# Kernel tuning notes

Hardware: AMD Instinct MI355X
Metric: run time of the kernel (lower is better)

Reference implementation:

```python
import jax, jax.numpy as jnp
import numpy as np

B, N, C, H, R = 16, 1024, 768, 12, 16
HD = C // H
SCALE = HD ** -0.5


def setup_inputs() -> dict:
    key = jax.random.key(0)
    ks = jax.random.split(key, 13)
    f = lambda k, shape, s=0.02: jax.random.normal(k, shape, dtype=jnp.float32) * s
    return {
        "x": jax.random.normal(ks[0], (B, N, C), dtype=jnp.float32),
        "W_qkv": f(ks[1], (3 * C, C)),
        "b_qkv": f(ks[2], (3 * C,)),
        "W_proj": f(ks[3], (C, C)),
        "b_proj": f(ks[4], (C,)),
        "A_q": f(ks[5], (R, C)),
        "B_q": f(ks[6], (C, R)),
        "A_k": f(ks[7], (R, C)),
        "B_k": f(ks[8], (C, R)),
        "A_v": f(ks[9], (R, C)),
        "B_v": f(ks[10], (C, R)),
        "A_o": f(ks[11], (R, C)),
        "B_o": f(ks[12], (C, R)),
    }


def _lora(x, A, Bu):
    # Adapter with no norm/act/bias, scaling=1.0: low-rank x @ A^T @ B^T
    return (x @ A.T) @ Bu.T


def _heads(t):
    # [B, N, C] -> [B, H, N, HD]
    return t.reshape(B, N, H, HD).transpose(0, 2, 1, 3)


def reference(x, W_qkv, b_qkv, W_proj, b_proj, A_q, B_q, A_k, B_k, A_v, B_v, A_o, B_o):
    qkv = x @ W_qkv.T + b_qkv                    # [B, N, 3C]
    qkv = qkv.reshape(B, N, 3, H, HD).transpose(2, 0, 3, 1, 4)  # [3, B, H, N, HD]
    q, k, v = qkv[0], qkv[1], qkv[2]
    q = q + _heads(_lora(x, A_q, B_q))
    k = k + _heads(_lora(x, A_k, B_k))
    v = v + _heads(_lora(x, A_v, B_v))
    attn = jnp.einsum("bhnd,bhmd->bhnm", q, k) * SCALE
    attn = jax.nn.softmax(attn, axis=-1)
    out = jnp.einsum("bhnm,bhmd->bhnd", attn, v)  # [B, H, N, HD]
    out = out.transpose(0, 2, 1, 3).reshape(B, N, C)
    out = out @ W_proj.T + b_proj
    out = out + _lora(out, A_o, B_o)
    return out
```

## Files before the change

kernel.cpp:

```cpp
#include <hip/hip_runtime.h>
#include <cmath>


#define DEVI __device__ __forceinline__

typedef float f32x4 __attribute__((ext_vector_type(4)));
typedef float f32x16 __attribute__((ext_vector_type(16)));
typedef short s16x8 __attribute__((ext_vector_type(8)));
typedef __bf16 b16x8 __attribute__((ext_vector_type(8)));
typedef unsigned int u32x4 __attribute__((ext_vector_type(4)));

static constexpr int MTOT = 16384;
static constexpr int C = 768;
static constexpr int N3 = 2304;

DEVI unsigned short f2bf(float x) {
  unsigned int u = __builtin_bit_cast(unsigned int, x);
  return (unsigned short)((u + 0x7FFFu + ((u >> 16) & 1u)) >> 16);
}

DEVI f32x4 mfma16(s16x8 a, s16x8 b, f32x4 c) {
  return __builtin_amdgcn_mfma_f32_16x16x32_bf16(
      __builtin_bit_cast(b16x8, a), __builtin_bit_cast(b16x8, b), c, 0, 0, 0);
}

DEVI f32x16 mfma32(s16x8 a, s16x8 b, f32x16 c) {
  return __builtin_amdgcn_mfma_f32_32x32x16_bf16(
      __builtin_bit_cast(b16x8, a), __builtin_bit_cast(b16x8, b), c, 0, 0, 0);
}

DEVI void async16(const void* g, void* l) {
  __builtin_amdgcn_global_load_lds(
      (__attribute__((address_space(1))) void*)g,
      (__attribute__((address_space(3))) void*)l, 16, 0, 0);
}

DEVI unsigned cvtpk_bf16(float lo, float hi2) {
  unsigned r;
  asm("v_cvt_pk_bf16_f32 %0, %1, %2" : "=v"(r) : "v"(lo), "v"(hi2));
  return r;
}


__global__ __launch_bounds__(256) void k_prep_x(const float* __restrict__ x,
                                                unsigned short* __restrict__ xb) {
  int idx = (blockIdx.x * 256 + threadIdx.x) * 4;
  float4 v = *(const float4*)(x + idx);
  uint2 p;
  p.x = (unsigned int)f2bf(v.x) | ((unsigned int)f2bf(v.y) << 16);
  p.y = (unsigned int)f2bf(v.z) | ((unsigned int)f2bf(v.w) << 16);
  *(uint2*)(xb + idx) = p;
}

__global__ __launch_bounds__(256) void k_prep_wqkv(
    const float* __restrict__ W, const float* __restrict__ Aq,
    const float* __restrict__ Bq, const float* __restrict__ Ak,
    const float* __restrict__ Bk, const float* __restrict__ Av,
    const float* __restrict__ Bv, unsigned short* __restrict__ out) {
  int idx = blockIdx.x * 256 + threadIdx.x;
  int n = idx / 768, c = idx - n * 768;
  int s = n / 768, co = n - s * 768;
  const float* A = (s == 0) ? Aq : (s == 1) ? Ak : Av;
  const float* Bm = (s == 0) ? Bq : (s == 1) ? Bk : Bv;
  float acc = W[idx];
#pragma unroll
  for (int r = 0; r < 16; ++r) acc += Bm[co * 16 + r] * A[r * 768 + c];
  out[idx] = f2bf(acc);
}

__global__ __launch_bounds__(256) void k_prep_M(const float* __restrict__ Ao,
                                                const float* __restrict__ Wp,
                                                float* __restrict__ M) {
  __shared__ float red[4][64];
  const int r = blockIdx.x, j0 = blockIdx.y * 64;
  const int jl = threadIdx.x & 63, cs = threadIdx.x >> 6;
  float acc = 0.f;
#pragma unroll 4
  for (int c = cs * 192; c < cs * 192 + 192; ++c)
    acc += Ao[r * 768 + c] * Wp[c * 768 + j0 + jl];
  red[cs][jl] = acc;
  __syncthreads();
  if (cs == 0)
    M[r * 768 + j0 + jl] = red[0][jl] + red[1][jl] + red[2][jl] + red[3][jl];
}

__global__ __launch_bounds__(256) void k_prep_wpe(const float* __restrict__ Wp,
                                                  const float* __restrict__ Bo,
                                                  const float* __restrict__ M,
                                                  unsigned short* __restrict__ out) {
  int idx = blockIdx.x * 256 + threadIdx.x;
  int n = idx / 768, j = idx - n * 768;
  float acc = Wp[idx];
#pragma unroll
  for (int r = 0; r < 16; ++r) acc += Bo[n * 16 + r] * M[r * 768 + j];
  out[idx] = f2bf(acc);
}

__global__ __launch_bounds__(256) void k_prep_beff(const float* __restrict__ bp,
                                                   const float* __restrict__ Ao,
                                                   const float* __restrict__ Bo,
                                                   float* __restrict__ beff) {
  __shared__ float red[256];
  __shared__ float bv[16];
  const int t = threadIdx.x;
  const int r = t >> 4, cs = t & 15;
  float a = 0.f;
#pragma unroll 4
  for (int c = cs * 48; c < cs * 48 + 48; ++c) a += Ao[r * 768 + c] * bp[c];
  red[t] = a;
  __syncthreads();
  if (cs == 0) {
    float s = 0.f;
#pragma unroll
    for (int k = 0; k < 16; ++k) s += red[r * 16 + k];
    bv[r] = s;
  }
  __syncthreads();
#pragma unroll
  for (int it = 0; it < 3; ++it) {
    const int n = it * 256 + t;
    float acc = bp[n];
#pragma unroll
    for (int r2 = 0; r2 < 16; ++r2) acc += Bo[n * 16 + r2] * bv[r2];
    beff[n] = acc;
  }
}


template <bool SWAP>
__global__ __launch_bounds__(256) void k_gemm_qkv_t(
    const unsigned short* __restrict__ A, const unsigned short* __restrict__ Bw,
    const float* __restrict__ bias, int nblk0, unsigned short* __restrict__ qb,
    unsigned short* __restrict__ kb, unsigned short* __restrict__ vtb) {
  __shared__ short la[2][128 * 32];
  __shared__ short lb[2][128 * 32];
  const int t = threadIdx.x;
  const int w = t >> 6, l = t & 63;
  const int i = l & 15, qd = l >> 4;
  const int wm = w >> 1, wn = w & 1;
  const int mblk = blockIdx.x, nblk = nblk0 + blockIdx.y;

  const unsigned short* Ab = A + (size_t)(mblk * 128) * 768;
  const unsigned short* Bb = Bw + (size_t)(nblk * 128) * 768;
  const int sr = l >> 2;
  const int sc = (l & 3) * 8;

  auto stage = [&](int bufn, int kb_) {
    const int k0 = kb_ * 32;
#pragma unroll
    for (int j = 0; j < 2; ++j) {
      const int row = w * 32 + j * 16 + sr;
      async16(Ab + row * 768 + k0 + sc, &la[bufn][(w * 32 + j * 16) * 32]);
      async16(Bb + row * 768 + k0 + sc, &lb[bufn][(w * 32 + j * 16) * 32]);
    }
  };

  stage(0, 0);

  f32x4 acc[4][4] = {};

  for (int kb_ = 0; kb_ < 24; ++kb_) {
    const int buf = kb_ & 1;
    __syncthreads();
    if (kb_ < 23) stage(buf ^ 1, kb_ + 1);
    s16x8 af[4], bf[4];
#pragma unroll
    for (int mi = 0; mi < 4; ++mi)
      af[mi] = *(const s16x8*)&la[buf][(wm * 64 + mi * 16 + i) * 32 + qd * 8];
#pragma unroll
    for (int ni = 0; ni < 4; ++ni)
      bf[ni] = *(const s16x8*)&lb[buf][(wn * 64 + ni * 16 + i) * 32 + qd * 8];
#pragma unroll
    for (int mi = 0; mi < 4; ++mi)
#pragma unroll
      for (int ni = 0; ni < 4; ++ni) {
        if constexpr (SWAP)
          acc[mi][ni] = mfma16(bf[ni], af[mi], acc[mi][ni]);
        else
          acc[mi][ni] = mfma16(af[mi], bf[ni], acc[mi][ni]);
      }
  }

  const float c1 = 0.18033688011112042f;
  if constexpr (SWAP) {
#pragma unroll
    for (int ni = 0; ni < 4; ++ni) {
      const int n0 = nblk * 128 + wn * 64 + ni * 16 + qd * 4;
      const int s = n0 / 768;
      const int nrel = n0 - s * 768;
      const int h = nrel >> 6, d0 = nrel & 63;
      const float4 bv4 = *(const float4*)(bias + n0);
      unsigned short* dst = (s == 0) ? qb : kb;
      const float scl = (s == 0) ? c1 : 1.0f;
#pragma unroll
      for (int mi = 0; mi < 4; ++mi) {
        const int m = mblk * 128 + wm * 64 + mi * 16 + i;
        const int b = m >> 10, pos = m & 1023;
        uint2 pk;
        pk.x = (unsigned int)f2bf((acc[mi][ni][0] + bv4.x) * scl) |
               ((unsigned int)f2bf((acc[mi][ni][1] + bv4.y) * scl) << 16);
        pk.y = (unsigned int)f2bf((acc[mi][ni][2] + bv4.z) * scl) |
               ((unsigned int)f2bf((acc[mi][ni][3] + bv4.w) * scl) << 16);
        *(uint2*)&dst[(size_t)((b * 12 + h) * 1024 + pos) * 64 + d0] = pk;
      }
    }
  } else {
#pragma unroll
    for (int ni = 0; ni < 4; ++ni) {
      const int n = nblk * 128 + wn * 64 + ni * 16 + i;
      const int nrel = n - 1536;
      const int h = nrel >> 6, d = nrel & 63;
      const float bvv = bias[n];
#pragma unroll
      for (int mi = 0; mi < 4; ++mi) {
        const int m0 = mblk * 128 + wm * 64 + mi * 16 + qd * 4;
        const int b = m0 >> 10, pos0 = m0 & 1023;
        uint2 pk;
        pk.x = (unsigned int)f2bf(acc[mi][ni][0] + bvv) |
               ((unsigned int)f2bf(acc[mi][ni][1] + bvv) << 16);
        pk.y = (unsigned int)f2bf(acc[mi][ni][2] + bvv) |
               ((unsigned int)f2bf(acc[mi][ni][3] + bvv) << 16);
        *(uint2*)&vtb[(size_t)((b * 12 + h) * 64 + d) * 1024 + pos0] = pk;
      }
    }
  }
}


__global__ __launch_bounds__(256, 4) void k_attn(
    const unsigned short* __restrict__ qg, const unsigned short* __restrict__ kg,
    const unsigned short* __restrict__ vtg, unsigned short* __restrict__ og) {
  __shared__ short k_lds[2][64 * 64];
  __shared__ short vt_lds[2][64 * 64];

  const int t = threadIdx.x;
  const int w = t >> 6, l = t & 63;
  const int lc = l & 31;
  const int hi = l >> 5;
  const int bh = blockIdx.x;
  const int qblk = blockIdx.y;
  const int h = bh % 12, b = bh / 12;

  const unsigned short* Qg = qg + (size_t)(bh * 1024 + qblk * 128) * 64;
  const unsigned short* Kg = kg + (size_t)bh * 1024 * 64;
  const unsigned short* Vtg = vtg + (size_t)bh * 64 * 1024;

  const int srl = l >> 3;
  const int sgc = (l & 7) ^ srl;

  s16x8 qf[4];
#pragma unroll
  for (int kc = 0; kc < 4; ++kc)
    qf[kc] = *(const s16x8*)(Qg + (w * 32 + lc) * 64 + kc * 16 + hi * 8);

  int koffs[2][4];
#pragma unroll
  for (int pg = 0; pg < 2; ++pg)
#pragma unroll
    for (int kc = 0; kc < 4; ++kc)
      koffs[pg][kc] = (pg * 32 + lc) * 64 + (((kc * 2 + hi) ^ (lc & 7)) * 8);
  int voffs[2][4][2];
#pragma unroll
  for (int nd = 0; nd < 2; ++nd)
#pragma unroll
    for (int mi = 0; mi < 4; ++mi)
#pragma unroll
      for (int h2 = 0; h2 < 2; ++h2)
        voffs[nd][mi][h2] =
            (nd * 32 + lc) * 64 + (((2 * mi + h2) ^ (lc & 7)) * 8) + 4 * hi;

  auto stage = [&](int bufn, int tkv) {
#pragma unroll
    for (int it = 0; it < 2; ++it) {
      const int rbase = it * 32 + w * 8;
      async16(Kg + (size_t)(tkv * 64 + rbase + srl) * 64 + sgc * 8,
              &k_lds[bufn][rbase * 64]);
      async16(Vtg + (size_t)(rbase + srl) * 1024 + tkv * 64 + sgc * 8,
              &vt_lds[bufn][rbase * 64]);
    }
  };

  stage(0, 0);

  f32x16 oacc[2] = {};
  float llocal = 0.f;

  for (int tkv = 0; tkv < 16; ++tkv) {
    const int buf = tkv & 1;
    __syncthreads();
    if (tkv < 15) stage(buf ^ 1, tkv + 1);

#pragma unroll
    for (int pg = 0; pg < 2; ++pg) {
      f32x16 st = {};
#pragma unroll
      for (int kc = 0; kc < 4; ++kc) {
        const s16x8 ka = *(const s16x8*)&k_lds[buf][koffs[pg][kc]];
        st = mfma32(ka, qf[kc], st);
      }
      unsigned pk[4][2];
#pragma unroll
      for (int q = 0; q < 4; ++q) {
        const float e0 = __builtin_amdgcn_exp2f(st[4 * q + 0]);
        const float e1 = __builtin_amdgcn_exp2f(st[4 * q + 1]);
        const float e2 = __builtin_amdgcn_exp2f(st[4 * q + 2]);
        const float e3 = __builtin_amdgcn_exp2f(st[4 * q + 3]);
        pk[q][0] = cvtpk_bf16(e0, e1);
        pk[q][1] = cvtpk_bf16(e2, e3);
        llocal += (e0 + e1) + (e2 + e3);
      }
      __builtin_amdgcn_s_setprio(1);
#pragma unroll
      for (int m = 0; m < 2; ++m) {
        const int mi = pg * 2 + m;
        u32x4 fa;
        fa[0] = pk[2 * m][0];
        fa[1] = pk[2 * m][1];
        fa[2] = pk[2 * m + 1][0];
        fa[3] = pk[2 * m + 1][1];
        const s16x8 paf = __builtin_bit_cast(s16x8, fa);
#pragma unroll
        for (int nd = 0; nd < 2; ++nd) {
          const uint2 vlo = *(const uint2*)&vt_lds[buf][voffs[nd][mi][0]];
          const uint2 vhi = *(const uint2*)&vt_lds[buf][voffs[nd][mi][1]];
          u32x4 vbu;
          vbu[0] = vlo.x;
          vbu[1] = vlo.y;
          vbu[2] = vhi.x;
          vbu[3] = vhi.y;
          oacc[nd] = mfma32(paf, __builtin_bit_cast(s16x8, vbu), oacc[nd]);
        }
      }
      __builtin_amdgcn_s_setprio(0);
    }
  }

  const float lq = llocal + __shfl_xor(llocal, 32, 64);
  float linv[16];
#pragma unroll
  for (int r = 0; r < 16; ++r)
    linv[r] = 1.0f / __shfl(lq, (r & 3) + 8 * (r >> 2) + 4 * hi, 64);

  const int orow0 = qblk * 128 + w * 32;
#pragma unroll
  for (int nd = 0; nd < 2; ++nd)
#pragma unroll
    for (int r = 0; r < 16; ++r) {
      const int pos = orow0 + (r & 3) + 8 * (r >> 2) + 4 * hi;
      const int d = nd * 32 + lc;
      og[(size_t)(b * 1024 + pos) * 768 + h * 64 + d] = f2bf(oacc[nd][r] * linv[r]);
    }
}


__global__ __launch_bounds__(256) void k_gemm_proj(
    const unsigned short* __restrict__ A, const unsigned short* __restrict__ Bw,
    const float* __restrict__ bias, float* __restrict__ out) {
  __shared__ short la[2][128 * 32];
  __shared__ short lb[2][128 * 32];
  const int t = threadIdx.x;
  const int w = t >> 6, l = t & 63;
  const int i = l & 15, qd = l >> 4;
  const int wm = w >> 1, wn = w & 1;
  const int mblk = blockIdx.x, nblk = blockIdx.y;

  const unsigned short* Ab = A + (size_t)(mblk * 128) * 768;
  const unsigned short* Bb = Bw + (size_t)(nblk * 128) * 768;
  const int sr = l >> 2;
  const int sc = (l & 3) * 8;

  auto stage = [&](int bufn, int kb_) {
    const int k0 = kb_ * 32;
#pragma unroll
    for (int j = 0; j < 2; ++j) {
      const int row = w * 32 + j * 16 + sr;
      async16(Ab + row * 768 + k0 + sc, &la[bufn][(w * 32 + j * 16) * 32]);
      async16(Bb + row * 768 + k0 + sc, &lb[bufn][(w * 32 + j * 16) * 32]);
    }
  };

  stage(0, 0);

  f32x4 acc[4][4] = {};

  for (int kb_ = 0; kb_ < 24; ++kb_) {
    const int buf = kb_ & 1;
    __syncthreads();
    if (kb_ < 23) stage(buf ^ 1, kb_ + 1);
    s16x8 af[4], bf[4];
#pragma unroll
    for (int mi = 0; mi < 4; ++mi)
      af[mi] = *(const s16x8*)&la[buf][(wm * 64 + mi * 16 + i) * 32 + qd * 8];
#pragma unroll
    for (int ni = 0; ni < 4; ++ni)
      bf[ni] = *(const s16x8*)&lb[buf][(wn * 64 + ni * 16 + i) * 32 + qd * 8];
#pragma unroll
    for (int mi = 0; mi < 4; ++mi)
#pragma unroll
      for (int ni = 0; ni < 4; ++ni)
        acc[mi][ni] = mfma16(bf[ni], af[mi], acc[mi][ni]);
  }

#pragma unroll
  for (int ni = 0; ni < 4; ++ni) {
    const int n0 = nblk * 128 + wn * 64 + ni * 16 + qd * 4;
    const float4 bv4 = *(const float4*)(bias + n0);
#pragma unroll
    for (int mi = 0; mi < 4; ++mi) {
      const int m = mblk * 128 + wm * 64 + mi * 16 + i;
      float4 o;
      o.x = acc[mi][ni][0] + bv4.x;
      o.y = acc[mi][ni][1] + bv4.y;
      o.z = acc[mi][ni][2] + bv4.z;
      o.w = acc[mi][ni][3] + bv4.w;
      *(float4*)&out[(size_t)m * 768 + n0] = o;
    }
  }
}


extern "C" void kernel_launch(void* const* d_in, const int* in_sizes, int n_in,
                              void* d_out, int out_size, void* d_ws, size_t ws_size,
                              hipStream_t stream) {
  const float* x = (const float*)d_in[0];
  const float* Wqkv = (const float*)d_in[1];
  const float* bqkv = (const float*)d_in[2];
  const float* Wp = (const float*)d_in[3];
  const float* bp = (const float*)d_in[4];
  const float* Aq = (const float*)d_in[5];
  const float* Bq = (const float*)d_in[6];
  const float* Ak = (const float*)d_in[7];
  const float* Bk = (const float*)d_in[8];
  const float* Av = (const float*)d_in[9];
  const float* Bv = (const float*)d_in[10];
  const float* Ao = (const float*)d_in[11];
  const float* Bo = (const float*)d_in[12];
  float* out = (float*)d_out;

  unsigned short* xb = (unsigned short*)d_ws;
  unsigned short* wqkvb = xb + (size_t)MTOT * C;
  unsigned short* wpeb = wqkvb + (size_t)N3 * C;
  unsigned short* qb = wpeb + (size_t)C * C;
  unsigned short* kb = qb + (size_t)MTOT * C;
  unsigned short* vtb = kb + (size_t)MTOT * C;
  float* Mbuf = (float*)(vtb + (size_t)MTOT * C);
  float* beff = Mbuf + 16 * 768;
  unsigned short* ob = xb;

  k_prep_x<<<12288, 256, 0, stream>>>(x, xb);
  k_prep_wqkv<<<6912, 256, 0, stream>>>(Wqkv, Aq, Bq, Ak, Bk, Av, Bv, wqkvb);
  k_prep_M<<<dim3(16, 12), 256, 0, stream>>>(Ao, Wp, Mbuf);
  k_prep_wpe<<<2304, 256, 0, stream>>>(Wp, Bo, Mbuf, wpeb);
  k_prep_beff<<<1, 256, 0, stream>>>(bp, Ao, Bo, beff);

  k_gemm_qkv_t<true><<<dim3(128, 12), 256, 0, stream>>>(xb, wqkvb, bqkv, 0,
                                                        qb, kb, vtb);
  k_gemm_qkv_t<false><<<dim3(128, 6), 256, 0, stream>>>(xb, wqkvb, bqkv, 12,
                                                        qb, kb, vtb);
  k_attn<<<dim3(192, 8), 256, 0, stream>>>(qb, kb, vtb, ob);
  k_gemm_proj<<<dim3(128, 6), 256, 0, stream>>>(ob, wpeb, beff, out);
}
```

Measured before the change: 367.4 us.

## Process two query tiles per attention block and merge QKV GEMM launches

Each attention workgroup now handles 256 query rows as two 128-row halves, so every K and V tile loaded into LDS feeds twice as many MFMAs. The grid shrinks to 192x4 and launch bounds drop to 2 waves per SIMD to leave room for the doubled accumulators and Q fragments. The two templated QKV GEMM launches are merged into one kernel that branches on blockIdx.y, removing a launch and a tail gap. The trade-off is higher register pressure and fewer resident blocks for the attention kernel.

```diff
diff --git a/kernel.cpp b/kernel.cpp
--- a/kernel.cpp
+++ b/kernel.cpp
@@ -128,17 +128,18 @@
 
 
 template <bool SWAP>
-__global__ __launch_bounds__(256) void k_gemm_qkv_t(
-    const unsigned short* __restrict__ A, const unsigned short* __restrict__ Bw,
-    const float* __restrict__ bias, int nblk0, unsigned short* __restrict__ qb,
-    unsigned short* __restrict__ kb, unsigned short* __restrict__ vtb) {
-  __shared__ short la[2][128 * 32];
-  __shared__ short lb[2][128 * 32];
+DEVI void qkv_body(const unsigned short* __restrict__ A,
+                   const unsigned short* __restrict__ Bw,
+                   const float* __restrict__ bias, int nblk,
+                   unsigned short* __restrict__ qb,
+                   unsigned short* __restrict__ kb,
+                   unsigned short* __restrict__ vtb,
+                   short (*la)[128 * 32], short (*lb)[128 * 32]) {
   const int t = threadIdx.x;
   const int w = t >> 6, l = t & 63;
   const int i = l & 15, qd = l >> 4;
   const int wm = w >> 1, wn = w & 1;
-  const int mblk = blockIdx.x, nblk = nblk0 + blockIdx.y;
+  const int mblk = blockIdx.x;
 
   const unsigned short* Ab = A + (size_t)(mblk * 128) * 768;
   const unsigned short* Bb = Bw + (size_t)(nblk * 128) * 768;
@@ -226,8 +227,20 @@
   }
 }
 
-
-__global__ __launch_bounds__(256, 4) void k_attn(
+__global__ __launch_bounds__(256) void k_gemm_qkv(
+    const unsigned short* __restrict__ A, const unsigned short* __restrict__ Bw,
+    const float* __restrict__ bias, unsigned short* __restrict__ qb,
+    unsigned short* __restrict__ kb, unsigned short* __restrict__ vtb) {
+  __shared__ short la[2][128 * 32];
+  __shared__ short lb[2][128 * 32];
+  if (blockIdx.y < 12)
+    qkv_body<true>(A, Bw, bias, blockIdx.y, qb, kb, vtb, la, lb);
+  else
+    qkv_body<false>(A, Bw, bias, blockIdx.y, qb, kb, vtb, la, lb);
+}
+
+
+__global__ __launch_bounds__(256, 2) void k_attn(
     const unsigned short* __restrict__ qg, const unsigned short* __restrict__ kg,
     const unsigned short* __restrict__ vtg, unsigned short* __restrict__ og) {
   __shared__ short k_lds[2][64 * 64];
@@ -238,20 +251,22 @@
   const int lc = l & 31;
   const int hi = l >> 5;
   const int bh = blockIdx.x;
-  const int qblk = blockIdx.y;
+  const int qpair = blockIdx.y;
   const int h = bh % 12, b = bh / 12;
 
-  const unsigned short* Qg = qg + (size_t)(bh * 1024 + qblk * 128) * 64;
+  const unsigned short* Qg = qg + (size_t)(bh * 1024 + qpair * 256) * 64;
   const unsigned short* Kg = kg + (size_t)bh * 1024 * 64;
   const unsigned short* Vtg = vtg + (size_t)bh * 64 * 1024;
 
   const int srl = l >> 3;
   const int sgc = (l & 7) ^ srl;
 
-  s16x8 qf[4];
-#pragma unroll
-  for (int kc = 0; kc < 4; ++kc)
-    qf[kc] = *(const s16x8*)(Qg + (w * 32 + lc) * 64 + kc * 16 + hi * 8);
+  s16x8 qfA[4], qfB[4];
+#pragma unroll
+  for (int kc = 0; kc < 4; ++kc) {
+    qfA[kc] = *(const s16x8*)(Qg + (w * 32 + lc) * 64 + kc * 16 + hi * 8);
+    qfB[kc] = *(const s16x8*)(Qg + (128 + w * 32 + lc) * 64 + kc * 16 + hi * 8);
+  }
 
   int koffs[2][4];
 #pragma unroll
@@ -282,8 +297,8 @@
 
   stage(0, 0);
 
-  f32x16 oacc[2] = {};
-  float llocal = 0.f;
+  f32x16 oaccA[2] = {}, oaccB[2] = {};
+  float llA = 0.f, llB = 0.f;
 
   for (int tkv = 0; tkv < 16; ++tkv) {
     const int buf = tkv & 1;
@@ -292,33 +307,49 @@
 
 #pragma unroll
     for (int pg = 0; pg < 2; ++pg) {
-      f32x16 st = {};
+      s16x8 ka[4];
+#pragma unroll
+      for (int kc = 0; kc < 4; ++kc)
+        ka[kc] = *(const s16x8*)&k_lds[buf][koffs[pg][kc]];
+      f32x16 stA = {}, stB = {};
 #pragma unroll
       for (int kc = 0; kc < 4; ++kc) {
-        const s16x8 ka = *(const s16x8*)&k_lds[buf][koffs[pg][kc]];
-        st = mfma32(ka, qf[kc], st);
-      }
-      unsigned pk[4][2];
+        stA = mfma32(ka[kc], qfA[kc], stA);
+        stB = mfma32(ka[kc], qfB[kc], stB);
+      }
+      unsigned pkA[4][2], pkB[4][2];
 #pragma unroll
       for (int q = 0; q < 4; ++q) {
-        const float e0 = __builtin_amdgcn_exp2f(st[4 * q + 0]);
-        const float e1 = __builtin_amdgcn_exp2f(st[4 * q + 1]);
-        const float e2 = __builtin_amdgcn_exp2f(st[4 * q + 2]);
-        const float e3 = __builtin_amdgcn_exp2f(st[4 * q + 3]);
-        pk[q][0] = cvtpk_bf16(e0, e1);
-        pk[q][1] = cvtpk_bf16(e2, e3);
-        llocal += (e0 + e1) + (e2 + e3);
+        const float a0 = __builtin_amdgcn_exp2f(stA[4 * q + 0]);
+        const float a1 = __builtin_amdgcn_exp2f(stA[4 * q + 1]);
+        const float a2 = __builtin_amdgcn_exp2f(stA[4 * q + 2]);
+        const float a3 = __builtin_amdgcn_exp2f(stA[4 * q + 3]);
+        pkA[q][0] = cvtpk_bf16(a0, a1);
+        pkA[q][1] = cvtpk_bf16(a2, a3);
+        llA += (a0 + a1) + (a2 + a3);
+        const float b0 = __builtin_amdgcn_exp2f(stB[4 * q + 0]);
+        const float b1 = __builtin_amdgcn_exp2f(stB[4 * q + 1]);
+        const float b2 = __builtin_amdgcn_exp2f(stB[4 * q + 2]);
+        const float b3 = __builtin_amdgcn_exp2f(stB[4 * q + 3]);
+        pkB[q][0] = cvtpk_bf16(b0, b1);
+        pkB[q][1] = cvtpk_bf16(b2, b3);
+        llB += (b0 + b1) + (b2 + b3);
       }
       __builtin_amdgcn_s_setprio(1);
 #pragma unroll
       for (int m = 0; m < 2; ++m) {
         const int mi = pg * 2 + m;
-        u32x4 fa;
-        fa[0] = pk[2 * m][0];
-        fa[1] = pk[2 * m][1];
-        fa[2] = pk[2 * m + 1][0];
-        fa[3] = pk[2 * m + 1][1];
-        const s16x8 paf = __builtin_bit_cast(s16x8, fa);
+        u32x4 faA, faB;
+        faA[0] = pkA[2 * m][0];
+        faA[1] = pkA[2 * m][1];
+        faA[2] = pkA[2 * m + 1][0];
+        faA[3] = pkA[2 * m + 1][1];
+        faB[0] = pkB[2 * m][0];
+        faB[1] = pkB[2 * m][1];
+        faB[2] = pkB[2 * m + 1][0];
+        faB[3] = pkB[2 * m + 1][1];
+        const s16x8 pafA = __builtin_bit_cast(s16x8, faA);
+        const s16x8 pafB = __builtin_bit_cast(s16x8, faB);
 #pragma unroll
         for (int nd = 0; nd < 2; ++nd) {
           const uint2 vlo = *(const uint2*)&vt_lds[buf][voffs[nd][mi][0]];
@@ -328,27 +359,36 @@
           vbu[1] = vlo.y;
           vbu[2] = vhi.x;
           vbu[3] = vhi.y;
-          oacc[nd] = mfma32(paf, __builtin_bit_cast(s16x8, vbu), oacc[nd]);
+          const s16x8 vb = __builtin_bit_cast(s16x8, vbu);
+          oaccA[nd] = mfma32(pafA, vb, oaccA[nd]);
+          oaccB[nd] = mfma32(pafB, vb, oaccB[nd]);
         }
       }
       __builtin_amdgcn_s_setprio(0);
     }
   }
 
-  const float lq = llocal + __shfl_xor(llocal, 32, 64);
-  float linv[16];
-#pragma unroll
-  for (int r = 0; r < 16; ++r)
-    linv[r] = 1.0f / __shfl(lq, (r & 3) + 8 * (r >> 2) + 4 * hi, 64);
-
-  const int orow0 = qblk * 128 + w * 32;
+  const float lqA = llA + __shfl_xor(llA, 32, 64);
+  const float lqB = llB + __shfl_xor(llB, 32, 64);
+  float linvA[16], linvB[16];
+#pragma unroll
+  for (int r = 0; r < 16; ++r) {
+    const int qr = (r & 3) + 8 * (r >> 2) + 4 * hi;
+    linvA[r] = 1.0f / __shfl(lqA, qr, 64);
+    linvB[r] = 1.0f / __shfl(lqB, qr, 64);
+  }
+
+  const int orow0 = qpair * 256 + w * 32;
 #pragma unroll
   for (int nd = 0; nd < 2; ++nd)
 #pragma unroll
     for (int r = 0; r < 16; ++r) {
-      const int pos = orow0 + (r & 3) + 8 * (r >> 2) + 4 * hi;
+      const int qr = (r & 3) + 8 * (r >> 2) + 4 * hi;
       const int d = nd * 32 + lc;
-      og[(size_t)(b * 1024 + pos) * 768 + h * 64 + d] = f2bf(oacc[nd][r] * linv[r]);
+      og[(size_t)(b * 1024 + orow0 + qr) * 768 + h * 64 + d] =
+          f2bf(oaccA[nd][r] * linvA[r]);
+      og[(size_t)(b * 1024 + orow0 + 128 + qr) * 768 + h * 64 + d] =
+          f2bf(oaccB[nd][r] * linvB[r]);
     }
 }
 
@@ -453,10 +493,7 @@
   k_prep_wpe<<<2304, 256, 0, stream>>>(Wp, Bo, Mbuf, wpeb);
   k_prep_beff<<<1, 256, 0, stream>>>(bp, Ao, Bo, beff);
 
-  k_gemm_qkv_t<true><<<dim3(128, 12), 256, 0, stream>>>(xb, wqkvb, bqkv, 0,
-                                                        qb, kb, vtb);
-  k_gemm_qkv_t<false><<<dim3(128, 6), 256, 0, stream>>>(xb, wqkvb, bqkv, 12,
-                                                        qb, kb, vtb);
-  k_attn<<<dim3(192, 8), 256, 0, stream>>>(qb, kb, vtb, ob);
+  k_gemm_qkv<<<dim3(128, 18), 256, 0, stream>>>(xb, wqkvb, bqkv, qb, kb, vtb);
+  k_attn<<<dim3(192, 4), 256, 0, stream>>>(qb, kb, vtb, ob);
   k_gemm_proj<<<dim3(128, 6), 256, 0, stream>>>(ob, wpeb, beff, out);
 }
```

New measurement: 350.3 us. 1.05x faster.
